# Kernel tuning notes

Hardware: AMD Instinct MI355X
Metric: run time of the kernel (lower is better)

The kernel has to match this reference:

```python
import jax, jax.numpy as jnp
import numpy as np

D_MODEL = 192
D_INNER = 384          # expand * d_model
D_STATE = 64
NHEADS = 8             # d_inner / headdim
HEADDIM = 48
D_CONV = 4
CONV_DIM = D_INNER + 2 * D_STATE   # 512 (ngroups=1)
D_IN_PROJ = 2 * D_INNER + 2 * D_STATE + NHEADS  # 904
MIX = 32
EPS = 1e-5


def silu(v):
    return v * jax.nn.sigmoid(v)


def setup_inputs() -> dict:
    key = jax.random.key(0)
    ks = jax.random.split(key, 16)
    B, L, C = 4, 4096, 4
    x = jax.random.normal(ks[0], (B, L, C), jnp.float32)
    Wfc = jax.random.normal(ks[1], (C, D_MODEL), jnp.float32) * 0.3
    bfc = jnp.zeros((D_MODEL,), jnp.float32)
    W_in = jax.random.normal(ks[2], (D_MODEL, D_IN_PROJ), jnp.float32) * 0.02
    conv_w = jax.random.normal(ks[3], (D_CONV, 1, CONV_DIM), jnp.float32) * 0.2  # depthwise (W,I/g,O)
    conv_b = jnp.zeros((CONV_DIM,), jnp.float32)
    # dt_bias = inv_softplus(dt_init) with dt_init ~ U(1e-3, 0.1)
    dt_init = jax.random.uniform(ks[4], (NHEADS,), jnp.float32, 1e-3, 0.1)
    dt_bias = jnp.log(jnp.expm1(dt_init))
    A_log = jnp.log(jax.random.uniform(ks[5], (NHEADS,), jnp.float32, 1.0, 16.0))
    Dparam = jnp.ones((NHEADS,), jnp.float32)
    norm_w = jnp.ones((D_INNER,), jnp.float32)
    W_out = jax.random.normal(ks[6], (D_INNER, D_MODEL), jnp.float32) * 0.02
    W1 = jax.random.normal(ks[7], (D_MODEL, MIX), jnp.float32) * 0.05
    b1 = jnp.zeros((MIX,), jnp.float32)
    W2 = jax.random.normal(ks[8], (MIX, MIX), jnp.float32) * 0.1
    b2 = jnp.zeros((MIX,), jnp.float32)
    Wo = jax.random.normal(ks[9], (MIX, 1), jnp.float32) * 0.1
    bo = jnp.zeros((1,), jnp.float32)
    return {"x": x, "Wfc": Wfc, "bfc": bfc, "W_in": W_in, "conv_w": conv_w,
            "conv_b": conv_b, "dt_bias": dt_bias, "A_log": A_log, "Dparam": Dparam,
            "norm_w": norm_w, "W_out": W_out, "W1": W1, "b1": b1, "W2": W2,
            "b2": b2, "Wo": Wo, "bo": bo}


def _mamba2(h, W_in, conv_w, conv_b, dt_bias, A_log, Dparam, norm_w, W_out):
    B, L, _ = h.shape
    zxbcdt = h @ W_in                                    # (B,L,904)
    z = zxbcdt[..., :D_INNER]
    xBC = zxbcdt[..., D_INNER:D_INNER + CONV_DIM]
    dt = jax.nn.softplus(zxbcdt[..., -NHEADS:] + dt_bias)  # (B,L,H)
    # causal depthwise conv1d
    xBC = jnp.pad(xBC, ((0, 0), (D_CONV - 1, 0), (0, 0)))
    xBC = jax.lax.conv_general_dilated(
        xBC, conv_w, window_strides=(1,), padding="VALID",
        dimension_numbers=("NWC", "WIO", "NWC"), feature_group_count=CONV_DIM)
    xBC = silu(xBC + conv_b)                             # (B,L,512)
    xs = xBC[..., :D_INNER].reshape(B, L, NHEADS, HEADDIM)
    Bm = xBC[..., D_INNER:D_INNER + D_STATE]             # (B,L,N)
    Cm = xBC[..., D_INNER + D_STATE:]                    # (B,L,N)
    A = -jnp.exp(A_log)                                  # (H,)
    dA = jnp.exp(dt * A)                                 # (B,L,H)

    def step(hstate, inp):
        dA_t, dt_t, B_t, x_t, C_t = inp                  # (B,H),(B,H),(B,N),(B,H,P),(B,N)
        dBx_t = jnp.einsum("bh,bn,bhp->bhpn", dt_t, B_t, x_t)
        hstate = dA_t[:, :, None, None] * hstate + dBx_t  # (B,H,P,N)
        y_t = jnp.einsum("bhpn,bn->bhp", hstate, C_t)
        return hstate, y_t

    h0 = jnp.zeros((B, NHEADS, HEADDIM, D_STATE), h.dtype)
    xs_t = jnp.swapaxes(xs, 0, 1)
    _, ys = jax.lax.scan(step, h0, (jnp.swapaxes(dA, 0, 1), jnp.swapaxes(dt, 0, 1),
                                    jnp.swapaxes(Bm, 0, 1), xs_t, jnp.swapaxes(Cm, 0, 1)))
    y = jnp.swapaxes(ys, 0, 1) + Dparam[None, None, :, None] * xs  # (B,L,H,P)
    y = y.reshape(B, L, D_INNER)
    # gated RMSNorm: rmsnorm(y * silu(z)) * weight
    y = y * silu(z)
    y = y * jax.lax.rsqrt(jnp.mean(y * y, axis=-1, keepdims=True) + EPS) * norm_w
    return y @ W_out                                     # (B,L,d_model)


def reference(x, Wfc, bfc, W_in, conv_w, conv_b, dt_bias, A_log, Dparam,
              norm_w, W_out, W1, b1, W2, b2, Wo, bo):
    h = x @ Wfc + bfc                                    # input_fc
    h = _mamba2(h, W_in, conv_w, conv_b, dt_bias, A_log, Dparam, norm_w, W_out)
    m = jax.nn.relu(h @ W1 + b1)
    m = jax.nn.relu(m @ W2 + b2)                         # dropout = identity (eval)
    m = jnp.mean(m, axis=1)                              # pool over time
    angle = (m @ Wo + bo)[:, 0]
    return angle
```

## Files before the change

kernel.cpp:

```cpp
#include <hip/hip_runtime.h>
#include <math.h>


#define BDIM 4
#define LDIM 4096
#define BL (BDIM*LDIM)
#define QC 64
#define NC (LDIM/QC)
#define BH (BDIM*NH)
#define NH 8

#define OFF_W    0u
#define OFF_Z    3145728u
#define OFF_T    9437184u
#define OFF_XS   17825792u
#define OFF_BM   24117248u
#define OFF_CM   25165824u
#define OFF_DT   26214400u
#define OFF_LAC  26345472u
#define OFF_SP   26476544u
#define OFF_Y    32768000u
#define OFF_MACC 39059456u

typedef unsigned short ushort_t;
typedef __attribute__((ext_vector_type(8))) short bf16x8;
typedef __attribute__((ext_vector_type(4))) float f32x4;

__device__ __forceinline__ float sigmoidf_(float x){ return 1.0f/(1.0f+__expf(-x)); }
__device__ __forceinline__ ushort_t f2bf(float x){
  unsigned int u = __float_as_uint(x);
  u += 0x7fffu + ((u>>16)&1u);
  return (ushort_t)(u>>16);
}
__device__ __forceinline__ float bf2f(ushort_t h){
  return __uint_as_float(((unsigned int)h)<<16);
}

__global__ void k_prep(const float* __restrict__ Wfc, const float* __restrict__ bfc,
                       const float* __restrict__ W_in, const float* __restrict__ W_out,
                       const float* __restrict__ W1, const float* __restrict__ norm_w,
                       float* __restrict__ Weff, float* __restrict__ beff,
                       float* __restrict__ Weff2, float* __restrict__ macc){
  int blk = blockIdx.x, tid = threadIdx.x;
  if (blk < 4){
    int n = blk*256 + tid;
    if (n >= 904) return;
    float a0=0.f,a1=0.f,a2=0.f,a3=0.f,ab=0.f;
    for (int d=0; d<192; d++){
      float w = W_in[(size_t)d*904 + n];
      a0 = fmaf(Wfc[d], w, a0);
      a1 = fmaf(Wfc[192+d], w, a1);
      a2 = fmaf(Wfc[384+d], w, a2);
      a3 = fmaf(Wfc[576+d], w, a3);
      ab = fmaf(bfc[d], w, ab);
    }
    Weff[n] = a0; Weff[904+n] = a1; Weff[1808+n] = a2; Weff[2712+n] = a3;
    beff[n] = ab;
  } else {
    if (blk == 4 && tid < 128) macc[tid] = 0.f;
    int g = (blk-4)*256 + tid;
    int i = g>>5, j = g&31;
    float a = 0.f;
    for (int d=0; d<192; d++) a = fmaf(W_out[(size_t)i*192+d], W1[d*32+j], a);
    Weff2[g] = a * norm_w[i];
  }
}

__global__ __launch_bounds__(256) void k_ipc(
    const float* __restrict__ x, const float* __restrict__ Weff,
    const float* __restrict__ beff, const float* __restrict__ conv_w,
    const float* __restrict__ conv_b, const float* __restrict__ dt_bias,
    ushort_t* __restrict__ xs_h, ushort_t* __restrict__ xs_l,
    ushort_t* __restrict__ Bm_h, ushort_t* __restrict__ Bm_l,
    ushort_t* __restrict__ Cm_h, ushort_t* __restrict__ Cm_l,
    float* __restrict__ dtb){
  __shared__ float sx[5][4];
  int pb = blockIdx.x, tid = threadIdx.x;
  int bl0 = pb*2;
  int l0 = bl0 & 4095, b = bl0 >> 12;
  if (tid < 20){
    int row = tid>>2, r = tid&3;
    int ll = l0-3+row;
    sx[row][r] = (ll>=0) ? x[(size_t)(b*4096+ll)*4 + r] : 0.f;
  }
  __syncthreads();
  if (tid < 16){
    int t = tid>>3, hh = tid&7;
    float raw = beff[896+hh];
    #pragma unroll
    for (int r=0;r<4;r++) raw = fmaf(sx[3+t][r], Weff[r*904+896+hh], raw);
    float xx = raw + dt_bias[hh];
    float dtv = (xx > 20.f) ? xx : log1pf(__expf(xx));
    dtb[(size_t)(b*8+hh)*4096 + l0 + t] = dtv;
  }
  #pragma unroll
  for (int half=0; half<2; half++){
    int c = tid + half*256;
    float w0 = Weff[384+c];
    float w1 = Weff[904+384+c];
    float w2 = Weff[1808+384+c];
    float w3 = Weff[2712+384+c];
    float bb = beff[384+c];
    float cw0 = conv_w[c], cw1 = conv_w[512+c], cw2 = conv_w[1024+c], cw3 = conv_w[1536+c];
    float cb = conv_b[c];
    float pre[5];
    #pragma unroll
    for (int q=0;q<5;q++){
      int ll = l0-3+q;
      float xv = bb;
      xv = fmaf(sx[q][0], w0, xv);
      xv = fmaf(sx[q][1], w1, xv);
      xv = fmaf(sx[q][2], w2, xv);
      xv = fmaf(sx[q][3], w3, xv);
      pre[q] = (ll >= 0) ? xv : 0.f;
    }
    float a0 = cb, a1 = cb;
    a0 = fmaf(cw0,pre[0],a0); a0 = fmaf(cw1,pre[1],a0);
    a0 = fmaf(cw2,pre[2],a0); a0 = fmaf(cw3,pre[3],a0);
    a1 = fmaf(cw0,pre[1],a1); a1 = fmaf(cw1,pre[2],a1);
    a1 = fmaf(cw2,pre[3],a1); a1 = fmaf(cw3,pre[4],a1);
    float v0 = a0 * sigmoidf_(a0);
    float v1 = a1 * sigmoidf_(a1);
    ushort_t h0 = f2bf(v0), lo0t = f2bf(v0 - bf2f(h0));
    ushort_t h1 = f2bf(v1), lo1t = f2bf(v1 - bf2f(h1));
    if (c < 384){
      int hh = c / 48, p = c - hh*48;
      size_t idx = (size_t)((b*8+hh)*4096 + l0)*48 + p;
      xs_h[idx] = h0; xs_l[idx] = lo0t;
      xs_h[idx+48] = h1; xs_l[idx+48] = lo1t;
    } else if (c < 448){
      size_t idx = (size_t)bl0*64 + (c-384);
      Bm_h[idx] = h0; Bm_l[idx] = lo0t;
      Bm_h[idx+64] = h1; Bm_l[idx+64] = lo1t;
    } else {
      size_t idx = (size_t)bl0*64 + (c-448);
      Cm_h[idx] = h0; Cm_l[idx] = lo0t;
      Cm_h[idx+64] = h1; Cm_l[idx+64] = lo1t;
    }
  }
}

__global__ __launch_bounds__(256, 3) void k_phase1(
    const float* __restrict__ dtbuf,
    const ushort_t* __restrict__ Bm_h, const ushort_t* __restrict__ Bm_l,
    const ushort_t* __restrict__ xs_h, const ushort_t* __restrict__ xs_l,
    const float* __restrict__ A_log,
    float* __restrict__ T, float* __restrict__ lac){
  __shared__ __align__(16) ushort_t sBh[64*72], sBl[64*72];
  __shared__ __align__(16) ushort_t sXh[48*72], sXl[48*72];
  __shared__ float sdt[64], sla[64], sw[64];
  int tid = threadIdx.x, blk = blockIdx.x;
  int bh = blk >> 6, k = blk & 63;
  int b = bh >> 3, hh = bh & 7;
  int t0 = k*64;
  int w = tid>>6, lane = tid&63, l15 = lane&15, quad = lane>>4;

  if (tid < 64) sdt[tid] = dtbuf[(size_t)bh*4096 + t0 + tid];
  __syncthreads();
  if (tid == 0){
    float eA = __expf(A_log[hh]);
    float cum = 0.f;
    for (int i=0;i<64;i++){ cum -= sdt[i]*eA; sla[i] = cum; }
  }
  __syncthreads();
  if (tid < 64){
    sw[tid] = __expf(sla[63]-sla[tid])*sdt[tid];
    lac[(size_t)blk*64 + tid] = sla[tid];
  }
  __syncthreads();
  {
    int s2 = (tid&31)*2, ng = (tid>>5)*8;
    size_t base0 = (size_t)(b*4096+t0+s2)*64 + ng;
    ushort_t h0a[8], l0a[8], h1a[8], l1a[8];
    *(uint4*)h0a = *(const uint4*)(Bm_h + base0);
    *(uint4*)l0a = *(const uint4*)(Bm_l + base0);
    *(uint4*)h1a = *(const uint4*)(Bm_h + base0 + 64);
    *(uint4*)l1a = *(const uint4*)(Bm_l + base0 + 64);
    float w0 = sw[s2], w1 = sw[s2+1];
    #pragma unroll
    for (int c=0;c<8;c++){
      float f0 = (bf2f(h0a[c]) + bf2f(l0a[c])) * w0;
      float f1 = (bf2f(h1a[c]) + bf2f(l1a[c])) * w1;
      ushort_t h0 = f2bf(f0), h1 = f2bf(f1);
      ushort_t lo0 = f2bf(f0-bf2f(h0)), lo1 = f2bf(f1-bf2f(h1));
      int o = (ng+c)*72 + s2;
      *(unsigned int*)&sBh[o] = (unsigned int)h0 | ((unsigned int)h1<<16);
      *(unsigned int*)&sBl[o] = (unsigned int)lo0 | ((unsigned int)lo1<<16);
    }
  }
  {
    int s2 = (tid>>3)*2, p0 = (tid&7)*6;
    const ushort_t* xh0 = xs_h + (size_t)(bh*4096+t0+s2)*48 + p0;
    const ushort_t* xl0 = xs_l + (size_t)(bh*4096+t0+s2)*48 + p0;
    #pragma unroll
    for (int c=0;c<6;c++){
      unsigned int hv = (unsigned int)xh0[c] | ((unsigned int)xh0[48+c]<<16);
      unsigned int lv = (unsigned int)xl0[c] | ((unsigned int)xl0[48+c]<<16);
      int o = (p0+c)*72 + s2;
      *(unsigned int*)&sXh[o] = hv;
      *(unsigned int*)&sXl[o] = lv;
    }
  }
  __syncthreads();
  f32x4 acc[3];
  #pragma unroll
  for (int t=0;t<3;t++) acc[t] = (f32x4)(0.f);
  #pragma unroll
  for (int ks=0;ks<2;ks++){
    int bo = (w*16+l15)*72 + ks*32 + quad*8;
    bf16x8 bbh = *(bf16x8*)&sBh[bo];
    bf16x8 bbl = *(bf16x8*)&sBl[bo];
    #pragma unroll
    for (int pt=0;pt<3;pt++){
      int xo = (pt*16+l15)*72 + ks*32 + quad*8;
      bf16x8 xah = *(bf16x8*)&sXh[xo];
      bf16x8 xal = *(bf16x8*)&sXl[xo];
      acc[pt] = __builtin_amdgcn_mfma_f32_16x16x32_bf16(xah, bbh, acc[pt], 0,0,0);
      acc[pt] = __builtin_amdgcn_mfma_f32_16x16x32_bf16(xah, bbl, acc[pt], 0,0,0);
      acc[pt] = __builtin_amdgcn_mfma_f32_16x16x32_bf16(xal, bbh, acc[pt], 0,0,0);
    }
  }
  {
    float* dst = T + (size_t)blk*3072;
    #pragma unroll
    for (int pt=0;pt<3;pt++)
      #pragma unroll
      for (int r=0;r<4;r++)
        dst[(pt*16+quad*4+r)*64 + w*16 + l15] = acc[pt][r];
  }
}

__global__ __launch_bounds__(256) void k_phase2p(
    const float* __restrict__ T, const float* __restrict__ lac,
    ushort_t* __restrict__ Sp_h, ushort_t* __restrict__ Sp_l){
  __shared__ __align__(16) float sT[64*64];
  __shared__ __align__(16) float sW[64][68];
  __shared__ float sc[64];
  int tid = threadIdx.x;
  int bh = blockIdx.x, es = blockIdx.y;
  #pragma unroll
  for (int r=0;r<4;r++){
    int idx = tid + r*256;
    int row = idx>>4, c4 = (idx&15)*4;
    *(float4*)&sT[row*64 + c4] = *(const float4*)(T + (size_t)(bh*64+row)*3072 + es*64 + c4);
  }
  if (tid < 64) sc[tid] = __expf(lac[(size_t)(bh*64+tid)*64 + 63]);
  __syncthreads();
  if (tid < 64){
    int k = tid;
    float w = 1.f;
    for (int j=63; j>=0; --j){
      bool a = (j < k);
      sW[j][k] = a ? w : 0.f;
      if (a) w *= sc[j];
    }
  }
  __syncthreads();
  int k0 = (tid>>4)*4, e0 = (tid&15)*4;
  float acc[4][4];
  #pragma unroll
  for (int i=0;i<4;i++)
    #pragma unroll
    for (int j=0;j<4;j++) acc[i][j]=0.f;
  int jmax = k0+2; if (jmax > 62) jmax = 62;
  for (int j=0; j<=jmax; ++j){
    float wv[4], tv[4];
    *(float4*)wv = *(float4*)&sW[j][k0];
    *(float4*)tv = *(float4*)&sT[j*64 + e0];
    #pragma unroll
    for (int i=0;i<4;i++)
      #pragma unroll
      for (int e=0;e<4;e++) acc[i][e] = fmaf(wv[i], tv[e], acc[i][e]);
  }
  #pragma unroll
  for (int i=0;i<4;i++){
    ushort4 h4, l4;
    ushort_t* hp = (ushort_t*)&h4;
    ushort_t* lp = (ushort_t*)&l4;
    #pragma unroll
    for (int e=0;e<4;e++){
      ushort_t hi = f2bf(acc[i][e]);
      hp[e] = hi;
      lp[e] = f2bf(acc[i][e] - bf2f(hi));
    }
    size_t o = (size_t)(bh*64+k0+i)*3072 + es*64 + e0;
    *(ushort4*)(Sp_h + o) = h4;
    *(ushort4*)(Sp_l + o) = l4;
  }
}

__global__ __launch_bounds__(256, 3) void k_phase3(
    const float* __restrict__ dtbuf, const float* __restrict__ lac,
    const ushort_t* __restrict__ Bm_h, const ushort_t* __restrict__ Bm_l,
    const ushort_t* __restrict__ Cm_h, const ushort_t* __restrict__ Cm_l,
    const ushort_t* __restrict__ xs_h, const ushort_t* __restrict__ xs_l,
    const ushort_t* __restrict__ Sp_h, const ushort_t* __restrict__ Sp_l,
    const float* __restrict__ Dparam, ushort_t* __restrict__ y16){
  __shared__ __align__(16) ushort_t sCh[64*72], sCl[64*72];
  __shared__ __align__(16) ushort_t sBh[64*72], sBl[64*72];
  __shared__ __align__(16) ushort_t sXh[48*72], sXl[48*72];
  __shared__ float sla[64], sdt[64];
  int tid = threadIdx.x, blk = blockIdx.x;
  int bh = blk>>6, k = blk&63, b = bh>>3, hh = bh&7, t0 = k*64;
  int w = tid>>6, lane = tid&63, l15 = lane&15, quad = lane>>4;

  if (tid < 64){
    sdt[tid] = dtbuf[(size_t)bh*4096 + t0 + tid];
    sla[tid] = lac[(size_t)blk*64 + tid];
  }
  {
    int row = tid>>2, ng = (tid&3)*16;
    size_t gb = (size_t)(b*4096+t0+row)*64 + ng;
    int o = row*72 + ng;
    *(uint4*)&sCh[o]   = *(const uint4*)(Cm_h + gb);
    *(uint4*)&sCh[o+8] = *(const uint4*)(Cm_h + gb + 8);
    *(uint4*)&sCl[o]   = *(const uint4*)(Cm_l + gb);
    *(uint4*)&sCl[o+8] = *(const uint4*)(Cm_l + gb + 8);
    *(uint4*)&sBh[o]   = *(const uint4*)(Bm_h + gb);
    *(uint4*)&sBh[o+8] = *(const uint4*)(Bm_h + gb + 8);
    *(uint4*)&sBl[o]   = *(const uint4*)(Bm_l + gb);
    *(uint4*)&sBl[o+8] = *(const uint4*)(Bm_l + gb + 8);
  }
  {
    int s2 = (tid>>3)*2, p0 = (tid&7)*6;
    const ushort_t* xh0 = xs_h + (size_t)(bh*4096+t0+s2)*48 + p0;
    const ushort_t* xl0 = xs_l + (size_t)(bh*4096+t0+s2)*48 + p0;
    #pragma unroll
    for (int c=0;c<6;c++){
      unsigned int hv = (unsigned int)xh0[c] | ((unsigned int)xh0[48+c]<<16);
      unsigned int lv = (unsigned int)xl0[c] | ((unsigned int)xl0[48+c]<<16);
      int o = (p0+c)*72 + s2;
      *(unsigned int*)&sXh[o] = hv;
      *(unsigned int*)&sXl[o] = lv;
    }
  }
  __syncthreads();

  f32x4 gacc[4];
  #pragma unroll
  for (int t=0;t<4;t++) gacc[t] = (f32x4)(0.f);
  {
    bf16x8 cah[2], cal[2];
    #pragma unroll
    for (int ks=0;ks<2;ks++){
      int ao = (w*16+l15)*72 + ks*32 + quad*8;
      cah[ks] = *(bf16x8*)&sCh[ao];
      cal[ks] = *(bf16x8*)&sCl[ao];
    }
    for (int bs=0; bs<=w; ++bs){
      #pragma unroll
      for (int ks=0;ks<2;ks++){
        int bo = (bs*16+l15)*72 + ks*32 + quad*8;
        bf16x8 bhf = *(bf16x8*)&sBh[bo];
        bf16x8 blf = *(bf16x8*)&sBl[bo];
        gacc[bs] = __builtin_amdgcn_mfma_f32_16x16x32_bf16(cah[ks], bhf, gacc[bs], 0,0,0);
        gacc[bs] = __builtin_amdgcn_mfma_f32_16x16x32_bf16(cah[ks], blf, gacc[bs], 0,0,0);
        gacc[bs] = __builtin_amdgcn_mfma_f32_16x16x32_bf16(cal[ks], bhf, gacc[bs], 0,0,0);
      }
    }
  }
  __syncthreads();

  for (int bs=0; bs<=w; ++bs){
    #pragma unroll
    for (int r=0;r<4;r++){
      int i = w*16 + quad*4 + r;
      int s = bs*16 + l15;
      float v = 0.f;
      if (s <= i) v = gacc[bs][r] * __expf(sla[i]-sla[s]) * sdt[s];
      ushort_t hi = f2bf(v);
      sBh[i*72+s] = hi;
      sBl[i*72+s] = f2bf(v - bf2f(hi));
    }
  }
  if (w==0){
    #pragma unroll
    for (int r=0;r<4;r++){ sBh[(quad*4+r)*72 + 16+l15] = 0; sBl[(quad*4+r)*72 + 16+l15] = 0; }
  }
  if (w==2){
    #pragma unroll
    for (int r=0;r<4;r++){ sBh[(32+quad*4+r)*72 + 48+l15] = 0; sBl[(32+quad*4+r)*72 + 48+l15] = 0; }
  }
  __syncthreads();

  bf16x8 pah[3][2], pal[3][2];
  {
    const ushort_t* sph = Sp_h + (size_t)blk*3072;
    const ushort_t* spl = Sp_l + (size_t)blk*3072;
    #pragma unroll
    for (int pt=0;pt<3;pt++)
      #pragma unroll
      for (int ks=0;ks<2;ks++){
        size_t o = (size_t)(pt*16+l15)*64 + ks*32 + quad*8;
        pah[pt][ks] = *(const bf16x8*)(sph + o);
        pal[pt][ks] = *(const bf16x8*)(spl + o);
      }
  }

  f32x4 accI[3], accA[3];
  #pragma unroll
  for (int t=0;t<3;t++){ accI[t] = (f32x4)(0.f); accA[t] = (f32x4)(0.f); }
  int nks = (w>=2) ? 2 : 1;
  for (int ks=0; ks<nks; ++ks){
    int go = (w*16+l15)*72 + ks*32 + quad*8;
    bf16x8 gbh = *(bf16x8*)&sBh[go];
    bf16x8 gbl = *(bf16x8*)&sBl[go];
    #pragma unroll
    for (int pt=0;pt<3;pt++){
      int xo = (pt*16+l15)*72 + ks*32 + quad*8;
      bf16x8 xah = *(bf16x8*)&sXh[xo];
      bf16x8 xal = *(bf16x8*)&sXl[xo];
      accI[pt] = __builtin_amdgcn_mfma_f32_16x16x32_bf16(xah, gbh, accI[pt], 0,0,0);
      accI[pt] = __builtin_amdgcn_mfma_f32_16x16x32_bf16(xah, gbl, accI[pt], 0,0,0);
      accI[pt] = __builtin_amdgcn_mfma_f32_16x16x32_bf16(xal, gbh, accI[pt], 0,0,0);
    }
  }
  #pragma unroll
  for (int ks=0; ks<2; ++ks){
    int co = (w*16+l15)*72 + ks*32 + quad*8;
    bf16x8 cbh = *(bf16x8*)&sCh[co];
    bf16x8 cbl = *(bf16x8*)&sCl[co];
    #pragma unroll
    for (int pt=0;pt<3;pt++){
      accA[pt] = __builtin_amdgcn_mfma_f32_16x16x32_bf16(pah[pt][ks], cbh, accA[pt], 0,0,0);
      accA[pt] = __builtin_amdgcn_mfma_f32_16x16x32_bf16(pah[pt][ks], cbl, accA[pt], 0,0,0);
      accA[pt] = __builtin_amdgcn_mfma_f32_16x16x32_bf16(pal[pt][ks], cbh, accA[pt], 0,0,0);
    }
  }
  {
    int i = w*16 + l15;
    float eli = __expf(sla[i]);
    float Dh = Dparam[hh];
    ushort_t* ybase = y16 + (size_t)(b*4096+t0+i)*384 + hh*48;
    #pragma unroll
    for (int pt=0;pt<3;pt++)
      #pragma unroll
      for (int r=0;r<4;r++){
        int p = pt*16 + quad*4 + r;
        float xf = bf2f(sXh[p*72 + i]) + bf2f(sXl[p*72 + i]);
        ybase[p] = f2bf(accI[pt][r] + eli*accA[pt][r] + Dh*xf);
      }
  }
}

__global__ __launch_bounds__(256) void k_gate(
    const float* __restrict__ x, const float* __restrict__ Weff,
    const float* __restrict__ beff,
    const ushort_t* __restrict__ y16, ushort_t* __restrict__ yn16){
  int tid = threadIdx.x;
  int w = tid>>6, lane = tid&63;
  int e0 = lane*6;
  float W0[6],W1v[6],W2v[6],W3v[6],bv[6];
  #pragma unroll
  for (int c=0;c<6;c++){
    int e = e0+c;
    W0[c]=Weff[e]; W1v[c]=Weff[904+e]; W2v[c]=Weff[1808+e]; W3v[c]=Weff[2712+e];
    bv[c]=beff[e];
  }
  #pragma unroll
  for (int t=0;t<4;t++){
    int bl = blockIdx.x*16 + w*4 + t;
    float4 xv = *(const float4*)(x + (size_t)bl*4);
    float g[6]; float ss = 0.f;
    #pragma unroll
    for (int c=0;c<6;c++){
      float zv = bv[c];
      zv = fmaf(xv.x, W0[c], zv);
      zv = fmaf(xv.y, W1v[c], zv);
      zv = fmaf(xv.z, W2v[c], zv);
      zv = fmaf(xv.w, W3v[c], zv);
      float yv = bf2f(y16[(size_t)bl*384 + e0 + c]);
      float gg = yv * (zv * sigmoidf_(zv));
      g[c] = gg; ss += gg*gg;
    }
    #pragma unroll
    for (int off=32; off>0; off>>=1) ss += __shfl_xor(ss, off);
    float rms = rsqrtf(ss*(1.f/384.f) + 1e-5f);
    #pragma unroll
    for (int c=0;c<6;c++)
      yn16[(size_t)bl*384 + e0 + c] = f2bf(g[c]*rms);
  }
}

__global__ __launch_bounds__(256) void k_mlp2(
    const ushort_t* __restrict__ yn16, const float* __restrict__ Weff2,
    const float* __restrict__ b1, const float* __restrict__ W2,
    const float* __restrict__ b2, float* __restrict__ macc){
  __shared__ __align__(16) float sW[384][32];
  __shared__ __align__(16) float sm1[64][33];
  __shared__ __align__(16) float sW2[32][32];
  __shared__ __align__(16) float sm2[64][33];
  int tid = threadIdx.x;
  int tok0 = blockIdx.x*64;
  int b = tok0 >> 12;
  #pragma unroll
  for (int r=0;r<12;r++){
    int idx = tid + r*256;
    int row = idx>>3, c4 = (idx&7)*4;
    *(float4*)&sW[row][c4] = *(const float4*)(Weff2 + (size_t)idx*4);
  }
  {
    int row = tid>>3, c4 = (tid&7)*4;
    *(float4*)&sW2[row][c4] = *(const float4*)(W2 + row*32 + c4);
  }
  __syncthreads();
  {
    int tk = tid>>3, j0 = (tid&7)*4;
    float a0[4], a1[4];
    #pragma unroll
    for (int j=0;j<4;j++){ a0[j] = b1[j0+j]; a1[j] = a0[j]; }
    const ushort_t* y0 = yn16 + (size_t)(tok0+tk)*384;
    const ushort_t* y1 = yn16 + (size_t)(tok0+tk+32)*384;
    for (int k8=0;k8<48;k8++){
      ushort_t ua[8], ub[8];
      *(uint4*)ua = *(const uint4*)(y0 + k8*8);
      *(uint4*)ub = *(const uint4*)(y1 + k8*8);
      #pragma unroll
      for (int c=0;c<8;c++){
        float va = bf2f(ua[c]), vb = bf2f(ub[c]);
        float w[4]; *(float4*)w = *(float4*)&sW[k8*8+c][j0];
        #pragma unroll
        for (int j=0;j<4;j++){ a0[j] = fmaf(va, w[j], a0[j]); a1[j] = fmaf(vb, w[j], a1[j]); }
      }
    }
    #pragma unroll
    for (int j=0;j<4;j++){
      sm1[tk][j0+j]    = fmaxf(a0[j], 0.f);
      sm1[tk+32][j0+j] = fmaxf(a1[j], 0.f);
    }
  }
  __syncthreads();
  {
    int tk = tid>>3, j0 = (tid&7)*4;
    float a0[4], a1[4];
    #pragma unroll
    for (int j=0;j<4;j++){ a0[j] = b2[j0+j]; a1[j] = a0[j]; }
    #pragma unroll
    for (int kk=0;kk<32;kk++){
      float va = sm1[tk][kk];
      float vb = sm1[tk+32][kk];
      float w[4]; *(float4*)w = *(float4*)&sW2[kk][j0];
      #pragma unroll
      for (int j=0;j<4;j++){ a0[j] = fmaf(va, w[j], a0[j]); a1[j] = fmaf(vb, w[j], a1[j]); }
    }
    #pragma unroll
    for (int j=0;j<4;j++){
      sm2[tk][j0+j]    = fmaxf(a0[j], 0.f);
      sm2[tk+32][j0+j] = fmaxf(a1[j], 0.f);
    }
  }
  __syncthreads();
  if (tid < 32){
    float t = 0.f;
    #pragma unroll
    for (int tok=0;tok<64;tok++) t += sm2[tok][tid];
    atomicAdd(&macc[b*32 + tid], t);
  }
}

__global__ void k_final(const float* __restrict__ macc, const float* __restrict__ Wo,
                        const float* __restrict__ bo, float* __restrict__ out){
  int tid = threadIdx.x;
  if (tid < 4){
    float acc = bo[0];
    #pragma unroll
    for (int j=0;j<32;j++) acc = fmaf(macc[tid*32+j]*(1.f/4096.f), Wo[j], acc);
    out[tid] = acc;
  }
}

extern "C" void kernel_launch(void* const* d_in, const int* in_sizes, int n_in,
                              void* d_out, int out_size, void* d_ws, size_t ws_size,
                              hipStream_t stream){
  const float* x      = (const float*)d_in[0];
  const float* Wfc    = (const float*)d_in[1];
  const float* bfc    = (const float*)d_in[2];
  const float* W_in   = (const float*)d_in[3];
  const float* conv_w = (const float*)d_in[4];
  const float* conv_b = (const float*)d_in[5];
  const float* dt_bias= (const float*)d_in[6];
  const float* A_log  = (const float*)d_in[7];
  const float* Dparam = (const float*)d_in[8];
  const float* norm_w = (const float*)d_in[9];
  const float* W_out  = (const float*)d_in[10];
  const float* W1     = (const float*)d_in[11];
  const float* b1     = (const float*)d_in[12];
  const float* W2     = (const float*)d_in[13];
  const float* b2     = (const float*)d_in[14];
  const float* Wo     = (const float*)d_in[15];
  const float* bo     = (const float*)d_in[16];
  float* ws  = (float*)d_ws;
  float* out = (float*)d_out;

  float* Weff  = ws + OFF_W;
  float* beff  = ws + OFF_W + 4096;
  float* Weff2 = ws + OFF_W + 8192;
  ushort_t* yn16 = (ushort_t*)(ws + OFF_Z);
  float* Tb    = ws + OFF_T;
  ushort_t* xs_h = (ushort_t*)(ws + OFF_XS);
  ushort_t* xs_l = xs_h + 6291456u;
  ushort_t* Bm_h = (ushort_t*)(ws + OFF_BM);
  ushort_t* Bm_l = Bm_h + 1048576u;
  ushort_t* Cm_h = (ushort_t*)(ws + OFF_CM);
  ushort_t* Cm_l = Cm_h + 1048576u;
  float* dtb   = ws + OFF_DT;
  float* lacb  = ws + OFF_LAC;
  ushort_t* Sp_h = (ushort_t*)(ws + OFF_SP);
  ushort_t* Sp_l = Sp_h + 6291456u;
  ushort_t* y16 = (ushort_t*)(ws + OFF_Y);
  float* macc  = ws + OFF_MACC;

  k_prep<<<dim3(52), dim3(256), 0, stream>>>(Wfc, bfc, W_in, W_out, W1, norm_w,
                                             Weff, beff, Weff2, macc);
  k_ipc<<<dim3(BL/2), dim3(256), 0, stream>>>(x, Weff, beff, conv_w, conv_b,
                                              dt_bias, xs_h, xs_l, Bm_h, Bm_l,
                                              Cm_h, Cm_l, dtb);
  k_phase1<<<dim3(BH*NC), dim3(256), 0, stream>>>(dtb, Bm_h, Bm_l, xs_h, xs_l,
                                                  A_log, Tb, lacb);
  k_phase2p<<<dim3(BH,48), dim3(256), 0, stream>>>(Tb, lacb, Sp_h, Sp_l);
  k_phase3<<<dim3(BH*NC), dim3(256), 0, stream>>>(dtb, lacb, Bm_h, Bm_l,
                                                  Cm_h, Cm_l, xs_h, xs_l,
                                                  Sp_h, Sp_l, Dparam, y16);
  k_gate<<<dim3(BL/16), dim3(256), 0, stream>>>(x, Weff, beff, y16, yn16);
  k_mlp2<<<dim3(BL/64), dim3(256), 0, stream>>>(yn16, Weff2, b1, W2, b2, macc);
  k_final<<<dim3(1), dim3(64), 0, stream>>>(macc, Wo, bo, out);
}
```

Measured before the change: 199.3 us.

## Drop low bf16 halves for chunk states and intra-chunk weights; widen conv per block

Chunk-state partials T are stored as bf16 instead of fp32, and the propagated states Sp keep only a single bf16 half instead of a hi/lo split. The intra-chunk G-weight matrix also drops its low half, which removes one MFMA per product in several places in phase3. k_ipc now computes four timesteps per block instead of two, halving its grid. The aim is less memory traffic and fewer MFMAs, at the cost of lower numerical precision in the scan.

```diff
diff --git a/kernel.cpp b/kernel.cpp
--- a/kernel.cpp
+++ b/kernel.cpp
@@ -74,17 +74,17 @@
     ushort_t* __restrict__ Bm_h, ushort_t* __restrict__ Bm_l,
     ushort_t* __restrict__ Cm_h, ushort_t* __restrict__ Cm_l,
     float* __restrict__ dtb){
-  __shared__ float sx[5][4];
+  __shared__ float sx[7][4];
   int pb = blockIdx.x, tid = threadIdx.x;
-  int bl0 = pb*2;
+  int bl0 = pb*4;
   int l0 = bl0 & 4095, b = bl0 >> 12;
-  if (tid < 20){
+  if (tid < 28){
     int row = tid>>2, r = tid&3;
     int ll = l0-3+row;
     sx[row][r] = (ll>=0) ? x[(size_t)(b*4096+ll)*4 + r] : 0.f;
   }
   __syncthreads();
-  if (tid < 16){
+  if (tid < 32){
     int t = tid>>3, hh = tid&7;
     float raw = beff[896+hh];
     #pragma unroll
@@ -103,9 +103,9 @@
     float bb = beff[384+c];
     float cw0 = conv_w[c], cw1 = conv_w[512+c], cw2 = conv_w[1024+c], cw3 = conv_w[1536+c];
     float cb = conv_b[c];
-    float pre[5];
-    #pragma unroll
-    for (int q=0;q<5;q++){
+    float pre[7];
+    #pragma unroll
+    for (int q=0;q<7;q++){
       int ll = l0-3+q;
       float xv = bb;
       xv = fmaf(sx[q][0], w0, xv);
@@ -114,28 +114,39 @@
       xv = fmaf(sx[q][3], w3, xv);
       pre[q] = (ll >= 0) ? xv : 0.f;
     }
-    float a0 = cb, a1 = cb;
-    a0 = fmaf(cw0,pre[0],a0); a0 = fmaf(cw1,pre[1],a0);
-    a0 = fmaf(cw2,pre[2],a0); a0 = fmaf(cw3,pre[3],a0);
-    a1 = fmaf(cw0,pre[1],a1); a1 = fmaf(cw1,pre[2],a1);
-    a1 = fmaf(cw2,pre[3],a1); a1 = fmaf(cw3,pre[4],a1);
-    float v0 = a0 * sigmoidf_(a0);
-    float v1 = a1 * sigmoidf_(a1);
-    ushort_t h0 = f2bf(v0), lo0t = f2bf(v0 - bf2f(h0));
-    ushort_t h1 = f2bf(v1), lo1t = f2bf(v1 - bf2f(h1));
+    float av[4];
+    #pragma unroll
+    for (int t=0;t<4;t++){
+      float a = cb;
+      a = fmaf(cw0,pre[t+0],a); a = fmaf(cw1,pre[t+1],a);
+      a = fmaf(cw2,pre[t+2],a); a = fmaf(cw3,pre[t+3],a);
+      av[t] = a * sigmoidf_(a);
+    }
     if (c < 384){
       int hh = c / 48, p = c - hh*48;
       size_t idx = (size_t)((b*8+hh)*4096 + l0)*48 + p;
-      xs_h[idx] = h0; xs_l[idx] = lo0t;
-      xs_h[idx+48] = h1; xs_l[idx+48] = lo1t;
+      #pragma unroll
+      for (int t=0;t<4;t++){
+        ushort_t h = f2bf(av[t]);
+        xs_h[idx + t*48] = h;
+        xs_l[idx + t*48] = f2bf(av[t] - bf2f(h));
+      }
     } else if (c < 448){
       size_t idx = (size_t)bl0*64 + (c-384);
-      Bm_h[idx] = h0; Bm_l[idx] = lo0t;
-      Bm_h[idx+64] = h1; Bm_l[idx+64] = lo1t;
+      #pragma unroll
+      for (int t=0;t<4;t++){
+        ushort_t h = f2bf(av[t]);
+        Bm_h[idx + t*64] = h;
+        Bm_l[idx + t*64] = f2bf(av[t] - bf2f(h));
+      }
     } else {
       size_t idx = (size_t)bl0*64 + (c-448);
-      Cm_h[idx] = h0; Cm_l[idx] = lo0t;
-      Cm_h[idx+64] = h1; Cm_l[idx+64] = lo1t;
+      #pragma unroll
+      for (int t=0;t<4;t++){
+        ushort_t h = f2bf(av[t]);
+        Cm_h[idx + t*64] = h;
+        Cm_l[idx + t*64] = f2bf(av[t] - bf2f(h));
+      }
     }
   }
 }
@@ -145,7 +156,7 @@
     const ushort_t* __restrict__ Bm_h, const ushort_t* __restrict__ Bm_l,
     const ushort_t* __restrict__ xs_h, const ushort_t* __restrict__ xs_l,
     const float* __restrict__ A_log,
-    float* __restrict__ T, float* __restrict__ lac){
+    ushort_t* __restrict__ T, float* __restrict__ lac){
   __shared__ __align__(16) ushort_t sBh[64*72], sBl[64*72];
   __shared__ __align__(16) ushort_t sXh[48*72], sXl[48*72];
   __shared__ float sdt[64], sla[64], sw[64];
@@ -221,28 +232,31 @@
     }
   }
   {
-    float* dst = T + (size_t)blk*3072;
+    ushort_t* dst = T + (size_t)blk*3072;
     #pragma unroll
     for (int pt=0;pt<3;pt++)
       #pragma unroll
       for (int r=0;r<4;r++)
-        dst[(pt*16+quad*4+r)*64 + w*16 + l15] = acc[pt][r];
+        dst[(pt*16+quad*4+r)*64 + w*16 + l15] = f2bf(acc[pt][r]);
   }
 }
 
 __global__ __launch_bounds__(256) void k_phase2p(
-    const float* __restrict__ T, const float* __restrict__ lac,
-    ushort_t* __restrict__ Sp_h, ushort_t* __restrict__ Sp_l){
+    const ushort_t* __restrict__ T, const float* __restrict__ lac,
+    ushort_t* __restrict__ Sp){
   __shared__ __align__(16) float sT[64*64];
   __shared__ __align__(16) float sW[64][68];
   __shared__ float sc[64];
   int tid = threadIdx.x;
   int bh = blockIdx.x, es = blockIdx.y;
   #pragma unroll
-  for (int r=0;r<4;r++){
+  for (int r=0;r<2;r++){
     int idx = tid + r*256;
-    int row = idx>>4, c4 = (idx&15)*4;
-    *(float4*)&sT[row*64 + c4] = *(const float4*)(T + (size_t)(bh*64+row)*3072 + es*64 + c4);
+    int row = idx>>3, g8 = (idx&7)*8;
+    ushort_t tv[8];
+    *(uint4*)tv = *(const uint4*)(T + (size_t)(bh*64+row)*3072 + es*64 + g8);
+    #pragma unroll
+    for (int c=0;c<8;c++) sT[row*64 + g8 + c] = bf2f(tv[c]);
   }
   if (tid < 64) sc[tid] = __expf(lac[(size_t)(bh*64+tid)*64 + 63]);
   __syncthreads();
@@ -274,18 +288,11 @@
   }
   #pragma unroll
   for (int i=0;i<4;i++){
-    ushort4 h4, l4;
+    ushort4 h4;
     ushort_t* hp = (ushort_t*)&h4;
-    ushort_t* lp = (ushort_t*)&l4;
-    #pragma unroll
-    for (int e=0;e<4;e++){
-      ushort_t hi = f2bf(acc[i][e]);
-      hp[e] = hi;
-      lp[e] = f2bf(acc[i][e] - bf2f(hi));
-    }
-    size_t o = (size_t)(bh*64+k0+i)*3072 + es*64 + e0;
-    *(ushort4*)(Sp_h + o) = h4;
-    *(ushort4*)(Sp_l + o) = l4;
+    #pragma unroll
+    for (int e=0;e<4;e++) hp[e] = f2bf(acc[i][e]);
+    *(ushort4*)(Sp + (size_t)(bh*64+k0+i)*3072 + es*64 + e0) = h4;
   }
 }
 
@@ -294,8 +301,8 @@
     const ushort_t* __restrict__ Bm_h, const ushort_t* __restrict__ Bm_l,
     const ushort_t* __restrict__ Cm_h, const ushort_t* __restrict__ Cm_l,
     const ushort_t* __restrict__ xs_h, const ushort_t* __restrict__ xs_l,
-    const ushort_t* __restrict__ Sp_h, const ushort_t* __restrict__ Sp_l,
-    const float* __restrict__ Dparam, ushort_t* __restrict__ y16){
+    const ushort_t* __restrict__ Sp, const float* __restrict__ Dparam,
+    ushort_t* __restrict__ y16){
   __shared__ __align__(16) ushort_t sCh[64*72], sCl[64*72];
   __shared__ __align__(16) ushort_t sBh[64*72], sBl[64*72];
   __shared__ __align__(16) ushort_t sXh[48*72], sXl[48*72];
@@ -368,33 +375,27 @@
       int s = bs*16 + l15;
       float v = 0.f;
       if (s <= i) v = gacc[bs][r] * __expf(sla[i]-sla[s]) * sdt[s];
-      ushort_t hi = f2bf(v);
-      sBh[i*72+s] = hi;
-      sBl[i*72+s] = f2bf(v - bf2f(hi));
+      sBh[i*72+s] = f2bf(v);
     }
   }
   if (w==0){
     #pragma unroll
-    for (int r=0;r<4;r++){ sBh[(quad*4+r)*72 + 16+l15] = 0; sBl[(quad*4+r)*72 + 16+l15] = 0; }
+    for (int r=0;r<4;r++) sBh[(quad*4+r)*72 + 16+l15] = 0;
   }
   if (w==2){
     #pragma unroll
-    for (int r=0;r<4;r++){ sBh[(32+quad*4+r)*72 + 48+l15] = 0; sBl[(32+quad*4+r)*72 + 48+l15] = 0; }
-  }
-  __syncthreads();
-
-  bf16x8 pah[3][2], pal[3][2];
-  {
-    const ushort_t* sph = Sp_h + (size_t)blk*3072;
-    const ushort_t* spl = Sp_l + (size_t)blk*3072;
+    for (int r=0;r<4;r++) sBh[(32+quad*4+r)*72 + 48+l15] = 0;
+  }
+  __syncthreads();
+
+  bf16x8 pah[3][2];
+  {
+    const ushort_t* sph = Sp + (size_t)blk*3072;
     #pragma unroll
     for (int pt=0;pt<3;pt++)
       #pragma unroll
-      for (int ks=0;ks<2;ks++){
-        size_t o = (size_t)(pt*16+l15)*64 + ks*32 + quad*8;
-        pah[pt][ks] = *(const bf16x8*)(sph + o);
-        pal[pt][ks] = *(const bf16x8*)(spl + o);
-      }
+      for (int ks=0;ks<2;ks++)
+        pah[pt][ks] = *(const bf16x8*)(sph + (size_t)(pt*16+l15)*64 + ks*32 + quad*8);
   }
 
   f32x4 accI[3], accA[3];
@@ -404,14 +405,12 @@
   for (int ks=0; ks<nks; ++ks){
     int go = (w*16+l15)*72 + ks*32 + quad*8;
     bf16x8 gbh = *(bf16x8*)&sBh[go];
-    bf16x8 gbl = *(bf16x8*)&sBl[go];
     #pragma unroll
     for (int pt=0;pt<3;pt++){
       int xo = (pt*16+l15)*72 + ks*32 + quad*8;
       bf16x8 xah = *(bf16x8*)&sXh[xo];
       bf16x8 xal = *(bf16x8*)&sXl[xo];
       accI[pt] = __builtin_amdgcn_mfma_f32_16x16x32_bf16(xah, gbh, accI[pt], 0,0,0);
-      accI[pt] = __builtin_amdgcn_mfma_f32_16x16x32_bf16(xah, gbl, accI[pt], 0,0,0);
       accI[pt] = __builtin_amdgcn_mfma_f32_16x16x32_bf16(xal, gbh, accI[pt], 0,0,0);
     }
   }
@@ -424,7 +423,6 @@
     for (int pt=0;pt<3;pt++){
       accA[pt] = __builtin_amdgcn_mfma_f32_16x16x32_bf16(pah[pt][ks], cbh, accA[pt], 0,0,0);
       accA[pt] = __builtin_amdgcn_mfma_f32_16x16x32_bf16(pah[pt][ks], cbl, accA[pt], 0,0,0);
-      accA[pt] = __builtin_amdgcn_mfma_f32_16x16x32_bf16(pal[pt][ks], cbh, accA[pt], 0,0,0);
     }
   }
   {
@@ -596,7 +594,7 @@
   float* beff  = ws + OFF_W + 4096;
   float* Weff2 = ws + OFF_W + 8192;
   ushort_t* yn16 = (ushort_t*)(ws + OFF_Z);
-  float* Tb    = ws + OFF_T;
+  ushort_t* Tb   = (ushort_t*)(ws + OFF_T);
   ushort_t* xs_h = (ushort_t*)(ws + OFF_XS);
   ushort_t* xs_l = xs_h + 6291456u;
   ushort_t* Bm_h = (ushort_t*)(ws + OFF_BM);
@@ -605,22 +603,21 @@
   ushort_t* Cm_l = Cm_h + 1048576u;
   float* dtb   = ws + OFF_DT;
   float* lacb  = ws + OFF_LAC;
-  ushort_t* Sp_h = (ushort_t*)(ws + OFF_SP);
-  ushort_t* Sp_l = Sp_h + 6291456u;
+  ushort_t* Spb  = (ushort_t*)(ws + OFF_SP);
   ushort_t* y16 = (ushort_t*)(ws + OFF_Y);
   float* macc  = ws + OFF_MACC;
 
   k_prep<<<dim3(52), dim3(256), 0, stream>>>(Wfc, bfc, W_in, W_out, W1, norm_w,
                                              Weff, beff, Weff2, macc);
-  k_ipc<<<dim3(BL/2), dim3(256), 0, stream>>>(x, Weff, beff, conv_w, conv_b,
+  k_ipc<<<dim3(BL/4), dim3(256), 0, stream>>>(x, Weff, beff, conv_w, conv_b,
                                               dt_bias, xs_h, xs_l, Bm_h, Bm_l,
                                               Cm_h, Cm_l, dtb);
   k_phase1<<<dim3(BH*NC), dim3(256), 0, stream>>>(dtb, Bm_h, Bm_l, xs_h, xs_l,
                                                   A_log, Tb, lacb);
-  k_phase2p<<<dim3(BH,48), dim3(256), 0, stream>>>(Tb, lacb, Sp_h, Sp_l);
+  k_phase2p<<<dim3(BH,48), dim3(256), 0, stream>>>(Tb, lacb, Spb);
   k_phase3<<<dim3(BH*NC), dim3(256), 0, stream>>>(dtb, lacb, Bm_h, Bm_l,
                                                   Cm_h, Cm_l, xs_h, xs_l,
-                                                  Sp_h, Sp_l, Dparam, y16);
+                                                  Spb, Dparam, y16);
   k_gate<<<dim3(BL/16), dim3(256), 0, stream>>>(x, Weff, beff, y16, yn16);
   k_mlp2<<<dim3(BL/64), dim3(256), 0, stream>>>(yn16, Weff2, b1, W2, b2, macc);
   k_final<<<dim3(1), dim3(64), 0, stream>>>(macc, Wo, bo, out);
```

New measurement: 189.5 us. -4.9%, faster.
